# Performance work log

Hardware: AMD Instinct MI355X
Metric: run time of the kernel (lower is better)

## Reference

```python
import jax, jax.numpy as jnp
import numpy as np

NUM_GRAPHS = 1024  # number of graphs in the batch (readout segments)


def setup_inputs() -> dict:
    key = jax.random.key(0)
    ks = jax.random.split(key, 10)
    N, F_IN, F1, F2, E = 100000, 64, 128, 64, 3200000
    x = jax.random.normal(ks[0], (N, F_IN), dtype=jnp.float32)
    adj = jax.random.randint(ks[1], (2, E), 0, N, dtype=jnp.int64)
    batch = jnp.sort(jax.random.randint(ks[2], (N,), 0, NUM_GRAPHS, dtype=jnp.int64))
    def xavier(k, shape):
        fan_in, fan_out = shape
        lim = jnp.sqrt(6.0 / (fan_in + fan_out))
        return jax.random.uniform(k, shape, jnp.float32, -lim, lim)
    W1 = xavier(ks[3], (F_IN, F1)); b1 = jax.random.uniform(ks[4], (F1,), jnp.float32)
    W2 = xavier(ks[5], (F1, F2));  b2 = jax.random.uniform(ks[6], (F2,), jnp.float32)
    Wm = xavier(ks[7], (2 * F2, F2)); bm = jax.random.uniform(ks[8], (F2,), jnp.float32)
    return {"x": x, "adj": adj, "batch": batch,
            "W1": W1, "b1": b1, "W2": W2, "b2": b2, "Wm": Wm, "bm": bm}


def _gcn_conv(x, W, b, src, dst):
    # GCNConv: out = D^{-1/2} (A + I) D^{-1/2} X W + b
    N = x.shape[0]
    h = x @ W  # [N, F_out]
    loops = jnp.arange(N, dtype=src.dtype)
    src_a = jnp.concatenate([src, loops])  # add self-loops
    dst_a = jnp.concatenate([dst, loops])
    deg = jax.ops.segment_sum(jnp.ones(src_a.shape[0], h.dtype), dst_a, num_segments=N)
    dinv = jax.lax.rsqrt(deg)  # deg >= 1 due to self-loops
    norm = dinv[src_a] * dinv[dst_a]  # [E+N]
    msg = h[src_a] * norm[:, None]    # gather + scale (memory-bound)
    return jax.ops.segment_sum(msg, dst_a, num_segments=N) + b


def _readout_meanmax(x, batch):
    G = NUM_GRAPHS
    s = jax.ops.segment_sum(x, batch, num_segments=G)
    cnt = jax.ops.segment_sum(jnp.ones(x.shape[0], x.dtype), batch, num_segments=G)
    mean = s / jnp.maximum(cnt, 1.0)[:, None]
    mx = jax.ops.segment_max(x, batch, num_segments=G)
    return jnp.concatenate([mean, mx], axis=1)  # [G, 2*F2]


def reference(x, adj, batch, W1, b1, W2, b2, Wm, bm):
    src, dst = adj[0], adj[1]
    h = jax.nn.relu(_gcn_conv(x, W1, b1, src, dst))
    h = _gcn_conv(h, W2, b2, src, dst)
    r = _readout_meanmax(h, batch)
    return r @ Wm + bm
```

## Files before the change

### kernel.cpp

```cpp
#include <hip/hip_runtime.h>
#include <hip/hip_fp16.h>
#include <cstdint>
#include <cstddef>

#define NGRAPH 1024
#define CHUNK 8192
#define SCTHREADS 512
#define SCIT (CHUNK / SCTHREADS)
#define MAXB 512
#define CAP 16384

typedef _Float16 f16x8 __attribute__((ext_vector_type(8)));
typedef float f32x4 __attribute__((ext_vector_type(4)));


__global__ __launch_bounds__(SCTHREADS) void scatter1_kernel(const int* __restrict__ src,
        const int* __restrict__ dst, int E, int B,
        int* __restrict__ bcnt, unsigned* __restrict__ ebuck,
        const float* __restrict__ W1, const float* __restrict__ W2,
        __half* __restrict__ W1s, __half* __restrict__ W2s,
        const int* __restrict__ batch, int N, int* __restrict__ goff) {
    __shared__ unsigned sorted[CHUNK];
    __shared__ int h[MAXB];
    __shared__ int lo[MAXB];
    __shared__ int cur[MAXB];
    __shared__ int gbase[MAXB];
    int blk = blockIdx.x, tid = threadIdx.x;
    int base = blk * CHUNK;
    int cnt_i = E - base; if (cnt_i > CHUNK) cnt_i = CHUNK;

    h[tid] = 0;
    __syncthreads();

    unsigned rd[SCIT], rs[SCIT];
    #pragma unroll
    for (int it = 0; it < SCIT; ++it) {
        int i = base + tid + it * SCTHREADS;
        if (i < E) {
            rd[it] = (unsigned)dst[i];
            rs[it] = (unsigned)src[i];
            atomicAdd(&h[rd[it] >> 8], 1);
        } else rd[it] = 0xFFFFFFFFu;
    }
    __syncthreads();

    int hv = h[tid];
    if (tid < B) gbase[tid] = hv ? atomicAdd(&bcnt[tid], hv) : 0;

    for (int o = 1; o < SCTHREADS; o <<= 1) {
        int t = (tid >= o) ? h[tid - o] : 0;
        __syncthreads();
        h[tid] += t;
        __syncthreads();
    }
    int excl = h[tid] - hv;
    lo[tid] = excl;
    cur[tid] = excl;
    __syncthreads();

    #pragma unroll
    for (int it = 0; it < SCIT; ++it) {
        if (rd[it] != 0xFFFFFFFFu) {
            int b = rd[it] >> 8;
            int p = atomicAdd(&cur[b], 1);
            sorted[p] = ((rd[it] & 255u) << 24) | rs[it];
        }
    }
    __syncthreads();

    for (int j = tid; j < cnt_i; j += SCTHREADS) {
        int l = (int)(((long long)j * B) / cnt_i);
        if (l > B - 1) l = B - 1;
        while (lo[l] > j) --l;
        while (l + 1 < B && lo[l + 1] <= j) ++l;
        ebuck[(size_t)l * CAP + gbase[l] + (j - lo[l])] = sorted[j];
    }

    if (blk == 0) {
        #pragma unroll
        for (int it = 0; it < 2; ++it) {
            int s = tid + it * SCTHREADS;
            int n = s & 15, q = (s >> 4) & 3, nt = (s >> 6) & 7, ks = s >> 9;
            int k0 = ks * 32 + q * 8, col = nt * 16 + n;
            __align__(16) __half hh[8];
            #pragma unroll
            for (int j = 0; j < 8; ++j) hh[j] = (__half)W1[(k0 + j) * 128 + col];
            *((uint4*)&W1s[(size_t)s * 8]) = *(uint4*)hh;
        }
        #pragma unroll
        for (int it = 0; it < 2; ++it) {
            int s = tid + it * SCTHREADS;
            int n = s & 15, q = (s >> 4) & 3, n2 = (s >> 6) & 3, ks2 = s >> 8;
            int k0 = ks2 * 32 + q * 8, col = n2 * 16 + n;
            __align__(16) __half hh[8];
            #pragma unroll
            for (int j = 0; j < 8; ++j) hh[j] = (__half)W2[(k0 + j) * 64 + col];
            *((uint4*)&W2s[(size_t)s * 8]) = *(uint4*)hh;
        }
    } else if (blk <= 2) {
        int g = (blk - 1) * SCTHREADS + tid;
        if (g < NGRAPH) {
            int lo2 = 0, hi2 = N;
            while (lo2 < hi2) {
                int mid = (lo2 + hi2) >> 1;
                if (batch[mid] < g) lo2 = mid + 1; else hi2 = mid;
            }
            goff[g] = lo2;
        }
        if (blk == 1 && tid == 0) goff[NGRAPH] = N;
    }
}

__global__ __launch_bounds__(256) void fine_kernel(const unsigned* __restrict__ ebuck,
        const int* __restrict__ bcnt, const float* __restrict__ x, int N, int B,
        int* __restrict__ row_beg, int* __restrict__ row_end, float* __restrict__ dinv,
        int* __restrict__ esrc, __half* __restrict__ xs) {
    __shared__ int hcnt[256];
    __shared__ int sc[256];
    __shared__ int loff[256];
    __shared__ float sdinv[256];
    int b = blockIdx.x, tid = threadIdx.x;
    int beg = b * CAP;
    int cnt = bcnt[b];
    hcnt[tid] = 0;
    __syncthreads();
    for (int e = tid; e < cnt; e += 256)
        atomicAdd(&hcnt[ebuck[beg + e] >> 24], 1);
    __syncthreads();
    int v = hcnt[tid];
    sc[tid] = v; __syncthreads();
    for (int o = 1; o < 256; o <<= 1) {
        int t = (tid >= o) ? sc[tid - o] : 0;
        __syncthreads();
        sc[tid] += t;
        __syncthreads();
    }
    int excl = sc[tid] - v;
    int n = (b << 8) + tid;
    float d = rsqrtf((float)(v + 1));
    if (n < N) {
        row_beg[n] = beg + excl;
        row_end[n] = beg + excl + v;
        dinv[n] = d;
    }
    loff[tid] = excl;
    sdinv[tid] = d;
    __syncthreads();
    for (int e = tid; e < cnt; e += 256) {
        unsigned u = ebuck[beg + e];
        int p = atomicAdd(&loff[u >> 24], 1);
        esrc[beg + p] = (int)(u & 0xFFFFFF);
    }
    const float4* xr = (const float4*)x;
    #pragma unroll
    for (int it = 0; it < 16; ++it) {
        int j = tid + it * 256;
        int node = j >> 4, cc = j & 15;
        int gn = (b << 8) + node;
        if (gn < N) {
            float dd = sdinv[node];
            float4 vv = xr[(size_t)gn * 16 + cc];
            __half2 h0 = __floats2half2_rn(vv.x * dd, vv.y * dd);
            __half2 h1 = __floats2half2_rn(vv.z * dd, vv.w * dd);
            uint2 u;
            u.x = *(unsigned*)&h0;
            u.y = *(unsigned*)&h1;
            ((uint2*)xs)[(size_t)gn * 16 + cc] = u;
        }
    }
}

__device__ inline void acc8h(__half2* a, const uint4& u) {
    const __half2* h = (const __half2*)&u;
    #pragma unroll
    for (int i = 0; i < 4; ++i) a[i] = __hadd2(a[i], h[i]);
}

__global__ __launch_bounds__(1024) void agg1_mlp_kernel(const __half* __restrict__ xs,
        const int* __restrict__ esrc, const int* __restrict__ row_beg,
        const int* __restrict__ row_end, const float* __restrict__ dinv,
        const __half* __restrict__ W1s, const __half* __restrict__ W2s,
        const float* __restrict__ b1, __half* __restrict__ T, int N) {
    __shared__ __align__(16) __half aggt[64][72];
    __shared__ __align__(16) __half h1t[4][16][136];
    int tid = threadIdx.x;
    int w = tid >> 6, lane = tid & 63;
    int g = lane >> 3, c = lane & 7;
    const uint4* xs4 = (const uint4*)xs;

    #pragma unroll
    for (int r = 0; r < 4; ++r) {
        int j = w * 4 + r;
        int n = blockIdx.x * 64 + j;
        if (n < N) {
            int beg = row_beg[n], end = row_end[n];
            __half2 ha[4] = {}, hb[4] = {};
            if (g == 0) acc8h(ha, xs4[(size_t)n * 8 + c]);
            int e = beg + g;
            for (; e + 8 < end; e += 16) {
                int s0 = esrc[e], s1 = esrc[e + 8];
                uint4 u0 = xs4[(size_t)s0 * 8 + c];
                uint4 u1 = xs4[(size_t)s1 * 8 + c];
                acc8h(ha, u0);
                acc8h(hb, u1);
            }
            if (e < end) acc8h(ha, xs4[(size_t)esrc[e] * 8 + c]);
            float a[8];
            #pragma unroll
            for (int i = 0; i < 4; ++i) {
                float2 fa = __half22float2(ha[i]), fb = __half22float2(hb[i]);
                a[2 * i]     = fa.x + fb.x;
                a[2 * i + 1] = fa.y + fb.y;
            }
            #pragma unroll
            for (int i = 0; i < 8; ++i) {
                a[i] += __shfl_xor(a[i], 8, 64);
                a[i] += __shfl_xor(a[i], 16, 64);
                a[i] += __shfl_xor(a[i], 32, 64);
            }
            if (g == 0) {
                float d = dinv[n];
                __align__(16) __half2 h[4];
                #pragma unroll
                for (int i = 0; i < 4; ++i)
                    h[i] = __floats2half2_rn(a[2 * i] * d, a[2 * i + 1] * d);
                *((uint4*)&aggt[j][c * 8]) = *(uint4*)h;
            }
        } else if (g == 0) {
            *((uint4*)&aggt[j][c * 8]) = make_uint4(0, 0, 0, 0);
        }
    }
    __syncthreads();

    if (w >= 4) return;
    int n15 = lane & 15, q = lane >> 4;
    int base = blockIdx.x * 64 + w * 16;
    f16x8 a10 = *(f16x8*)&aggt[w * 16 + n15][q * 8];
    f16x8 a11 = *(f16x8*)&aggt[w * 16 + n15][32 + q * 8];
    const uint4* W1f = (const uint4*)W1s;
    #pragma unroll
    for (int nt = 0; nt < 8; ++nt) {
        f32x4 cc = {0.f, 0.f, 0.f, 0.f};
        uint4 ub0 = W1f[(nt * 4 + q) * 16 + n15];
        uint4 ub1 = W1f[((8 + nt) * 4 + q) * 16 + n15];
        cc = __builtin_amdgcn_mfma_f32_16x16x32_f16(a10, *(f16x8*)&ub0, cc, 0, 0, 0);
        cc = __builtin_amdgcn_mfma_f32_16x16x32_f16(a11, *(f16x8*)&ub1, cc, 0, 0, 0);
        float bv = b1[nt * 16 + n15];
        #pragma unroll
        for (int rr = 0; rr < 4; ++rr) {
            float hv = fmaxf(cc[rr] + bv, 0.f);
            h1t[w][q * 4 + rr][nt * 16 + n15] = (__half)hv;
        }
    }
    f16x8 a2[4];
    #pragma unroll
    for (int ks2 = 0; ks2 < 4; ++ks2)
        a2[ks2] = *(f16x8*)&h1t[w][n15][ks2 * 32 + q * 8];
    const uint4* W2f = (const uint4*)W2s;
    #pragma unroll
    for (int n2 = 0; n2 < 4; ++n2) {
        f32x4 cc = {0.f, 0.f, 0.f, 0.f};
        #pragma unroll
        for (int ks2 = 0; ks2 < 4; ++ks2) {
            uint4 ub = W2f[((ks2 * 4 + n2) * 4 + q) * 16 + n15];
            cc = __builtin_amdgcn_mfma_f32_16x16x32_f16(a2[ks2], *(f16x8*)&ub, cc, 0, 0, 0);
        }
        #pragma unroll
        for (int rr = 0; rr < 4; ++rr) {
            int node = base + q * 4 + rr;
            if (node < N) {
                float v = cc[rr] * dinv[node];
                T[(size_t)node * 64 + n2 * 16 + n15] = (__half)v;
            }
        }
    }
}

__global__ __launch_bounds__(256) void agg_h2f_kernel(const __half* __restrict__ xs,
        const int* __restrict__ esrc, const int* __restrict__ row_beg,
        const int* __restrict__ row_end, const float* __restrict__ dinv,
        const float* __restrict__ bias, float* __restrict__ out, int N) {
    int n = blockIdx.x * 4 + (threadIdx.x >> 6);
    if (n >= N) return;
    int lane = threadIdx.x & 63;
    int g = lane >> 3, c = lane & 7;
    const uint4* xs4 = (const uint4*)xs;
    int beg = row_beg[n], end = row_end[n];
    __half2 ha[4] = {}, hb[4] = {};
    if (g == 0) acc8h(ha, xs4[(size_t)n * 8 + c]);
    int e = beg + g;
    for (; e + 8 < end; e += 16) {
        int s0 = esrc[e], s1 = esrc[e + 8];
        uint4 u0 = xs4[(size_t)s0 * 8 + c];
        uint4 u1 = xs4[(size_t)s1 * 8 + c];
        acc8h(ha, u0);
        acc8h(hb, u1);
    }
    if (e < end) acc8h(ha, xs4[(size_t)esrc[e] * 8 + c]);
    float a[8];
    #pragma unroll
    for (int i = 0; i < 4; ++i) {
        float2 fa = __half22float2(ha[i]), fb = __half22float2(hb[i]);
        a[2 * i]     = fa.x + fb.x;
        a[2 * i + 1] = fa.y + fb.y;
    }
    #pragma unroll
    for (int i = 0; i < 8; ++i) {
        a[i] += __shfl_xor(a[i], 8, 64);
        a[i] += __shfl_xor(a[i], 16, 64);
        a[i] += __shfl_xor(a[i], 32, 64);
    }
    if (g == 0) {
        float d = dinv[n];
        float4 bb0 = ((const float4*)bias)[c * 2];
        float4 bb1 = ((const float4*)bias)[c * 2 + 1];
        float4 o0, o1;
        o0.x = a[0] * d + bb0.x; o0.y = a[1] * d + bb0.y;
        o0.z = a[2] * d + bb0.z; o0.w = a[3] * d + bb0.w;
        o1.x = a[4] * d + bb1.x; o1.y = a[5] * d + bb1.y;
        o1.z = a[6] * d + bb1.z; o1.w = a[7] * d + bb1.w;
        ((float4*)out)[(size_t)n * 16 + c * 2] = o0;
        ((float4*)out)[(size_t)n * 16 + c * 2 + 1] = o1;
    }
}

__global__ __launch_bounds__(256) void readout_head_kernel(const float* __restrict__ h2,
        const int* __restrict__ goff, const float* __restrict__ Wm,
        const float* __restrict__ bm, float* __restrict__ out) {
    int g = blockIdx.x;
    int beg = goff[g], end = goff[g + 1];
    int f = threadIdx.x & 63;
    int c = threadIdx.x >> 6;
    float s = 0.f, m = -3.4e38f;
    for (int n = beg + c; n < end; n += 4) {
        float v = h2[(size_t)n * 64 + f];
        s += v;
        m = fmaxf(m, v);
    }
    __shared__ float ss[4][64], sm[4][64];
    __shared__ float rr[128];
    ss[c][f] = s; sm[c][f] = m;
    __syncthreads();
    if (c == 0) {
        float S = ss[0][f] + ss[1][f] + ss[2][f] + ss[3][f];
        float M = fmaxf(fmaxf(sm[0][f], sm[1][f]), fmaxf(sm[2][f], sm[3][f]));
        int cnt = end - beg;
        rr[f] = (cnt > 0) ? S / (float)cnt : 0.f;
        rr[64 + f] = (cnt > 0) ? M : 0.f;
    }
    __syncthreads();
    if (threadIdx.x < 64) {
        int j = threadIdx.x;
        float acc = bm[j];
        #pragma unroll 4
        for (int k = 0; k < 128; ++k)
            acc = fmaf(rr[k], Wm[k * 64 + j], acc);
        out[(size_t)g * 64 + j] = acc;
    }
}

extern "C" void kernel_launch(void* const* d_in, const int* in_sizes, int n_in,
                              void* d_out, int out_size, void* d_ws, size_t ws_size,
                              hipStream_t stream) {
    const float* x    = (const float*)d_in[0];
    const int*  adj   = (const int*)d_in[1];
    const int*  batch = (const int*)d_in[2];
    const float* W1   = (const float*)d_in[3];
    const float* b1   = (const float*)d_in[4];
    const float* W2   = (const float*)d_in[5];
    const float* b2   = (const float*)d_in[6];
    const float* Wm   = (const float*)d_in[7];
    const float* bm   = (const float*)d_in[8];
    float* out = (float*)d_out;

    const int N = in_sizes[0] / 64;
    const int E = in_sizes[1] / 2;
    const int* src = adj;
    const int* dst = adj + E;
    const int B = (N + 255) >> 8;
    const int nblocks = (E + CHUNK - 1) / CHUNK;

    char* w = (char*)d_ws;
    size_t off = 0;
    auto carve = [&](size_t bytes) -> void* {
        void* p = w + off;
        off += (bytes + 255) & ~(size_t)255;
        return p;
    };
    size_t halfbuf = (size_t)N * 64 * 2;
    float* dinv    = (float*)carve((size_t)N * 4);
    int*   row_beg = (int*)  carve((size_t)N * 4);
    int*   row_end = (int*)  carve((size_t)N * 4);
    int*   esrc    = (int*)  carve((size_t)B * CAP * 4);
    unsigned* ebuck= (unsigned*)carve((size_t)B * CAP * 4);
    int*   bcnt    = (int*)  carve((MAXB + 1) * 4);
    int*   goff    = (int*)  carve((NGRAPH + 1) * 4);
    __half* W1s    = (__half*)carve(8192 * 2);
    __half* W2s    = (__half*)carve(8192 * 2);
    __half* xs_h   = (__half*)carve(halfbuf);
    __half* ts_h   = (__half*)carve(halfbuf);
    float* h2      = (float*)carve((size_t)N * 64 * 4);

    hipMemsetAsync(bcnt, 0, (MAXB + 1) * 4, stream);

    scatter1_kernel<<<nblocks, SCTHREADS, 0, stream>>>(src, dst, E, B, bcnt, ebuck,
                                                       W1, W2, W1s, W2s, batch, N, goff);
    fine_kernel<<<B, 256, 0, stream>>>(ebuck, bcnt, x, N, B, row_beg, row_end,
                                       dinv, esrc, xs_h);

    agg1_mlp_kernel<<<(N + 63) / 64, 1024, 0, stream>>>(xs_h, esrc, row_beg, row_end,
                                                        dinv, W1s, W2s, b1, ts_h, N);

    agg_h2f_kernel<<<(N + 3) / 4, 256, 0, stream>>>(ts_h, esrc, row_beg, row_end,
                                                    dinv, b2, h2, N);

    readout_head_kernel<<<NGRAPH, 256, 0, stream>>>(h2, goff, Wm, bm, out);
}
```

Before: 332.2 us.

## Split layer-1 aggregation from the fused MLP into separate kernels

Splits the combined aggregation+MLP kernel (1024-thread blocks where only 4 of 16 waves ran the MFMA stage) into a 256-thread gather-aggregate kernel writing fp16 aggregates to global memory, followed by a separate fused two-layer MFMA MLP kernel. The aim is to improve occupancy and scheduling of the memory-bound gather by removing the large shared-memory footprint and idle waves. The cost is an extra global round-trip of an N×64 fp16 buffer and one more kernel launch. The MLP output reuses the xs buffer.

```diff
diff --git a/kernel.cpp b/kernel.cpp
--- a/kernel.cpp
+++ b/kernel.cpp
@@ -176,103 +176,47 @@
     for (int i = 0; i < 4; ++i) a[i] = __hadd2(a[i], h[i]);
 }
 
-__global__ __launch_bounds__(1024) void agg1_mlp_kernel(const __half* __restrict__ xs,
+__global__ __launch_bounds__(256) void agg_h2h_kernel(const __half* __restrict__ xs,
         const int* __restrict__ esrc, const int* __restrict__ row_beg,
         const int* __restrict__ row_end, const float* __restrict__ dinv,
-        const __half* __restrict__ W1s, const __half* __restrict__ W2s,
-        const float* __restrict__ b1, __half* __restrict__ T, int N) {
-    __shared__ __align__(16) __half aggt[64][72];
-    __shared__ __align__(16) __half h1t[4][16][136];
-    int tid = threadIdx.x;
-    int w = tid >> 6, lane = tid & 63;
+        __half* __restrict__ out, int N) {
+    int n = blockIdx.x * 4 + (threadIdx.x >> 6);
+    if (n >= N) return;
+    int lane = threadIdx.x & 63;
     int g = lane >> 3, c = lane & 7;
     const uint4* xs4 = (const uint4*)xs;
-
-    #pragma unroll
-    for (int r = 0; r < 4; ++r) {
-        int j = w * 4 + r;
-        int n = blockIdx.x * 64 + j;
-        if (n < N) {
-            int beg = row_beg[n], end = row_end[n];
-            __half2 ha[4] = {}, hb[4] = {};
-            if (g == 0) acc8h(ha, xs4[(size_t)n * 8 + c]);
-            int e = beg + g;
-            for (; e + 8 < end; e += 16) {
-                int s0 = esrc[e], s1 = esrc[e + 8];
-                uint4 u0 = xs4[(size_t)s0 * 8 + c];
-                uint4 u1 = xs4[(size_t)s1 * 8 + c];
-                acc8h(ha, u0);
-                acc8h(hb, u1);
-            }
-            if (e < end) acc8h(ha, xs4[(size_t)esrc[e] * 8 + c]);
-            float a[8];
-            #pragma unroll
-            for (int i = 0; i < 4; ++i) {
-                float2 fa = __half22float2(ha[i]), fb = __half22float2(hb[i]);
-                a[2 * i]     = fa.x + fb.x;
-                a[2 * i + 1] = fa.y + fb.y;
-            }
-            #pragma unroll
-            for (int i = 0; i < 8; ++i) {
-                a[i] += __shfl_xor(a[i], 8, 64);
-                a[i] += __shfl_xor(a[i], 16, 64);
-                a[i] += __shfl_xor(a[i], 32, 64);
-            }
-            if (g == 0) {
-                float d = dinv[n];
-                __align__(16) __half2 h[4];
-                #pragma unroll
-                for (int i = 0; i < 4; ++i)
-                    h[i] = __floats2half2_rn(a[2 * i] * d, a[2 * i + 1] * d);
-                *((uint4*)&aggt[j][c * 8]) = *(uint4*)h;
-            }
-        } else if (g == 0) {
-            *((uint4*)&aggt[j][c * 8]) = make_uint4(0, 0, 0, 0);
-        }
-    }
-    __syncthreads();
-
-    if (w >= 4) return;
-    int n15 = lane & 15, q = lane >> 4;
-    int base = blockIdx.x * 64 + w * 16;
-    f16x8 a10 = *(f16x8*)&aggt[w * 16 + n15][q * 8];
-    f16x8 a11 = *(f16x8*)&aggt[w * 16 + n15][32 + q * 8];
-    const uint4* W1f = (const uint4*)W1s;
-    #pragma unroll
-    for (int nt = 0; nt < 8; ++nt) {
-        f32x4 cc = {0.f, 0.f, 0.f, 0.f};
-        uint4 ub0 = W1f[(nt * 4 + q) * 16 + n15];
-        uint4 ub1 = W1f[((8 + nt) * 4 + q) * 16 + n15];
-        cc = __builtin_amdgcn_mfma_f32_16x16x32_f16(a10, *(f16x8*)&ub0, cc, 0, 0, 0);
-        cc = __builtin_amdgcn_mfma_f32_16x16x32_f16(a11, *(f16x8*)&ub1, cc, 0, 0, 0);
-        float bv = b1[nt * 16 + n15];
-        #pragma unroll
-        for (int rr = 0; rr < 4; ++rr) {
-            float hv = fmaxf(cc[rr] + bv, 0.f);
-            h1t[w][q * 4 + rr][nt * 16 + n15] = (__half)hv;
-        }
-    }
-    f16x8 a2[4];
-    #pragma unroll
-    for (int ks2 = 0; ks2 < 4; ++ks2)
-        a2[ks2] = *(f16x8*)&h1t[w][n15][ks2 * 32 + q * 8];
-    const uint4* W2f = (const uint4*)W2s;
-    #pragma unroll
-    for (int n2 = 0; n2 < 4; ++n2) {
-        f32x4 cc = {0.f, 0.f, 0.f, 0.f};
-        #pragma unroll
-        for (int ks2 = 0; ks2 < 4; ++ks2) {
-            uint4 ub = W2f[((ks2 * 4 + n2) * 4 + q) * 16 + n15];
-            cc = __builtin_amdgcn_mfma_f32_16x16x32_f16(a2[ks2], *(f16x8*)&ub, cc, 0, 0, 0);
-        }
-        #pragma unroll
-        for (int rr = 0; rr < 4; ++rr) {
-            int node = base + q * 4 + rr;
-            if (node < N) {
-                float v = cc[rr] * dinv[node];
-                T[(size_t)node * 64 + n2 * 16 + n15] = (__half)v;
-            }
-        }
+    int beg = row_beg[n], end = row_end[n];
+    __half2 ha[4] = {}, hb[4] = {};
+    if (g == 0) acc8h(ha, xs4[(size_t)n * 8 + c]);
+    int e = beg + g;
+    for (; e + 8 < end; e += 16) {
+        int s0 = esrc[e], s1 = esrc[e + 8];
+        uint4 u0 = xs4[(size_t)s0 * 8 + c];
+        uint4 u1 = xs4[(size_t)s1 * 8 + c];
+        acc8h(ha, u0);
+        acc8h(hb, u1);
+    }
+    if (e < end) acc8h(ha, xs4[(size_t)esrc[e] * 8 + c]);
+    float a[8];
+    #pragma unroll
+    for (int i = 0; i < 4; ++i) {
+        float2 fa = __half22float2(ha[i]), fb = __half22float2(hb[i]);
+        a[2 * i]     = fa.x + fb.x;
+        a[2 * i + 1] = fa.y + fb.y;
+    }
+    #pragma unroll
+    for (int i = 0; i < 8; ++i) {
+        a[i] += __shfl_xor(a[i], 8, 64);
+        a[i] += __shfl_xor(a[i], 16, 64);
+        a[i] += __shfl_xor(a[i], 32, 64);
+    }
+    if (g == 0) {
+        float d = dinv[n];
+        __align__(16) __half2 h[4];
+        #pragma unroll
+        for (int i = 0; i < 4; ++i)
+            h[i] = __floats2half2_rn(a[2 * i] * d, a[2 * i + 1] * d);
+        ((uint4*)out)[(size_t)n * 8 + c] = *(uint4*)h;
     }
 }
 
@@ -324,6 +268,63 @@
     }
 }
 
+__global__ __launch_bounds__(256) void fusedmlp_kernel(const __half* __restrict__ A,
+        const __half* __restrict__ W1s, const __half* __restrict__ W2s,
+        const float* __restrict__ b1, const float* __restrict__ dinv,
+        __half* __restrict__ T, int N) {
+    __shared__ __align__(16) __half h1t[4][16][136];
+    int tid = threadIdx.x;
+    int w = tid >> 6, lane = tid & 63;
+    int n15 = lane & 15, q = lane >> 4;
+    int base = blockIdx.x * 64 + w * 16;
+
+    int m = base + n15; if (m >= N) m = N - 1;
+    const uint4* Ar = (const uint4*)(A + (size_t)m * 64);
+    uint4 ua0 = Ar[q];
+    uint4 ua1 = Ar[4 + q];
+    f16x8 a10 = *(f16x8*)&ua0;
+    f16x8 a11 = *(f16x8*)&ua1;
+    const uint4* W1f = (const uint4*)W1s;
+    #pragma unroll
+    for (int nt = 0; nt < 8; ++nt) {
+        f32x4 c = {0.f, 0.f, 0.f, 0.f};
+        uint4 ub0 = W1f[(nt * 4 + q) * 16 + n15];
+        uint4 ub1 = W1f[((8 + nt) * 4 + q) * 16 + n15];
+        c = __builtin_amdgcn_mfma_f32_16x16x32_f16(a10, *(f16x8*)&ub0, c, 0, 0, 0);
+        c = __builtin_amdgcn_mfma_f32_16x16x32_f16(a11, *(f16x8*)&ub1, c, 0, 0, 0);
+        float bv = b1[nt * 16 + n15];
+        #pragma unroll
+        for (int rr = 0; rr < 4; ++rr) {
+            float hv = fmaxf(c[rr] + bv, 0.f);
+            h1t[w][q * 4 + rr][nt * 16 + n15] = (__half)hv;
+        }
+    }
+    __syncthreads();
+
+    f16x8 a2[4];
+    #pragma unroll
+    for (int ks2 = 0; ks2 < 4; ++ks2)
+        a2[ks2] = *(f16x8*)&h1t[w][n15][ks2 * 32 + q * 8];
+    const uint4* W2f = (const uint4*)W2s;
+    #pragma unroll
+    for (int n2 = 0; n2 < 4; ++n2) {
+        f32x4 c = {0.f, 0.f, 0.f, 0.f};
+        #pragma unroll
+        for (int ks2 = 0; ks2 < 4; ++ks2) {
+            uint4 ub = W2f[((ks2 * 4 + n2) * 4 + q) * 16 + n15];
+            c = __builtin_amdgcn_mfma_f32_16x16x32_f16(a2[ks2], *(f16x8*)&ub, c, 0, 0, 0);
+        }
+        #pragma unroll
+        for (int rr = 0; rr < 4; ++rr) {
+            int node = base + q * 4 + rr;
+            if (node < N) {
+                float v = c[rr] * dinv[node];
+                T[(size_t)node * 64 + n2 * 16 + n15] = (__half)v;
+            }
+        }
+    }
+}
+
 __global__ __launch_bounds__(256) void readout_head_kernel(const float* __restrict__ h2,
         const int* __restrict__ goff, const float* __restrict__ Wm,
         const float* __restrict__ bm, float* __restrict__ out) {
@@ -398,8 +399,9 @@
     __half* W1s    = (__half*)carve(8192 * 2);
     __half* W2s    = (__half*)carve(8192 * 2);
     __half* xs_h   = (__half*)carve(halfbuf);
-    __half* ts_h   = (__half*)carve(halfbuf);
+    __half* agg1h  = (__half*)carve(halfbuf);
     float* h2      = (float*)carve((size_t)N * 64 * 4);
+    __half* ts_h = xs_h;
 
     hipMemsetAsync(bcnt, 0, (MAXB + 1) * 4, stream);
 
@@ -408,8 +410,10 @@
     fine_kernel<<<B, 256, 0, stream>>>(ebuck, bcnt, x, N, B, row_beg, row_end,
                                        dinv, esrc, xs_h);
 
-    agg1_mlp_kernel<<<(N + 63) / 64, 1024, 0, stream>>>(xs_h, esrc, row_beg, row_end,
-                                                        dinv, W1s, W2s, b1, ts_h, N);
+    agg_h2h_kernel<<<(N + 3) / 4, 256, 0, stream>>>(xs_h, esrc, row_beg, row_end,
+                                                    dinv, agg1h, N);
+
+    fusedmlp_kernel<<<(N + 63) / 64, 256, 0, stream>>>(agg1h, W1s, W2s, b1, dinv, ts_h, N);
 
     agg_h2f_kernel<<<(N + 3) / 4, 256, 0, stream>>>(ts_h, esrc, row_beg, row_end,
                                                     dinv, b2, h2, N);
```

Measured after the change: 309.6 us. 6.8% less time.
